# Performance work log

Measured on AMD Instinct MI355X. Metric: run time of the kernel, lower is better.

Reference implementation:

```python
import jax, jax.numpy as jnp
import numpy as np

N = 50000


def gcn_conv(x, ei, W, b, n_nodes):
    """PyG GCNConv with default add_self_loops=True, symmetric normalization."""
    h = x @ W  # [N, hidden]
    loop = jnp.arange(n_nodes, dtype=ei.dtype)
    src = jnp.concatenate([ei[0], loop])
    dst = jnp.concatenate([ei[1], loop])
    # degree over destination nodes, unit edge weights (incl. self loops)
    deg = jax.ops.segment_sum(jnp.ones(src.shape[0], dtype=h.dtype), dst, num_segments=n_nodes)
    dinv = jnp.where(deg > 0, jax.lax.rsqrt(deg), 0.0)
    norm = dinv[src] * dinv[dst]  # [E+N]
    out = jax.ops.segment_sum(norm[:, None] * h[src], dst, num_segments=n_nodes)
    return out + b


def setup_inputs() -> dict:
    key = jax.random.key(0)
    ks = jax.random.split(key, 16)
    d_in, hidden, d_out, E = 64, 64, 3, 800000
    inp = {
        "x": jax.random.normal(ks[0], (N, d_in), dtype=jnp.float32),
        "ei_spring": jax.random.randint(ks[1], (2, E), 0, N, dtype=jnp.int32),
        "ei_damper": jax.random.randint(ks[2], (2, E), 0, N, dtype=jnp.int32),
        "W1s": jax.random.normal(ks[3], (d_in, hidden), dtype=jnp.float32) / np.sqrt(d_in),
        "b1s": jnp.zeros((hidden,), dtype=jnp.float32),
        "W1d": jax.random.normal(ks[4], (d_in, hidden), dtype=jnp.float32) / np.sqrt(d_in),
        "b1d": jnp.zeros((hidden,), dtype=jnp.float32),
        "W2s": jax.random.normal(ks[5], (hidden, hidden), dtype=jnp.float32) / np.sqrt(hidden),
        "b2s": jnp.zeros((hidden,), dtype=jnp.float32),
        "W2d": jax.random.normal(ks[6], (hidden, hidden), dtype=jnp.float32) / np.sqrt(hidden),
        "b2d": jnp.zeros((hidden,), dtype=jnp.float32),
        "Wlin": jax.random.normal(ks[7], (hidden, d_out), dtype=jnp.float32) / np.sqrt(hidden),
        "blin": jnp.zeros((d_out,), dtype=jnp.float32),
    }
    return inp


def reference(x, ei_spring, ei_damper, W1s, b1s, W1d, b1d, W2s, b2s, W2d, b2d, Wlin, blin):
    # layer 1: HeteroConv sum over both relations, then ReLU
    h = gcn_conv(x, ei_spring, W1s, b1s, N) + gcn_conv(x, ei_damper, W1d, b1d, N)
    h = jax.nn.relu(h)
    # layer 2
    h = gcn_conv(h, ei_spring, W2s, b2s, N) + gcn_conv(h, ei_damper, W2d, b2d, N)
    h = jax.nn.relu(h)
    return h @ Wlin + blin
```

## Files before the change

kernel.cpp:

```cpp
#include <hip/hip_runtime.h>
#include <hip/hip_fp16.h>

#define NN 50000
#define BSHIFT 8
#define NBK ((NN + 255) >> 8)
#define CHUNK 4096
#define CAP 8192

typedef __attribute__((ext_vector_type(8))) _Float16 f16x8;
typedef __attribute__((ext_vector_type(4))) float f32x4;

__device__ __forceinline__ float recw(unsigned r) {
    unsigned short us = (unsigned short)(r >> 16);
    __half h;
    __builtin_memcpy(&h, &us, 2);
    return __half2float(h);
}
__device__ __forceinline__ float2 h2f2(unsigned v) {
    __half2 h;
    __builtin_memcpy(&h, &v, 4);
    return __half22float2(h);
}
__device__ __forceinline__ unsigned f2h2(float a, float b) {
    __half2 h = __floats2half2_rn(a, b);
    unsigned u;
    __builtin_memcpy(&u, &h, 4);
    return u;
}
__device__ __forceinline__ f16x8 as_f16x8(uint4 v) {
    f16x8 r;
    __builtin_memcpy(&r, &v, 16);
    return r;
}
__device__ __forceinline__ unsigned short f2h1(float v) {
    __half h = __float2half(v);
    unsigned short us;
    __builtin_memcpy(&us, &h, 2);
    return us;
}


__global__ __launch_bounds__(256) void fat_prep(const int* __restrict__ eiS, int Es,
                                                const int* __restrict__ eiD, int Ed,
                                                int* __restrict__ cntS,
                                                int* __restrict__ cntD,
                                                const float* __restrict__ x,
                                                unsigned* __restrict__ x16, int total4,
                                                const float* __restrict__ W1s,
                                                const float* __restrict__ W1d,
                                                const float* __restrict__ W2s,
                                                const float* __restrict__ W2d,
                                                unsigned short* __restrict__ Bp) {
    __shared__ int h[NBK];
    if (blockIdx.y < 2) {
        int rel = blockIdx.y;
        const int* dst = rel ? (eiD + Ed) : (eiS + Es);
        int E = rel ? Ed : Es;
        int* cnt = rel ? cntD : cntS;
        int base = blockIdx.x * CHUNK;
        if (base >= E) return;
        for (int i = threadIdx.x; i < NBK; i += 256) h[i] = 0;
        __syncthreads();
        int end = (base + CHUNK < E) ? base + CHUNK : E;
        for (int e = base + threadIdx.x; e < end; e += 256)
            atomicAdd(&h[dst[e] >> BSHIFT], 1);
        __syncthreads();
        for (int i = threadIdx.x; i < NBK; i += 256)
            if (h[i]) atomicAdd(&cnt[i], h[i]);
    } else {
        int i = blockIdx.x * 256 + threadIdx.x;
        if (i < total4) {
            float4 v = reinterpret_cast<const float4*>(x)[i];
            uint2 o;
            o.x = f2h2(v.x, v.y);
            o.y = f2h2(v.z, v.w);
            reinterpret_cast<uint2*>(x16)[i] = o;
        }
        if (blockIdx.x < 64) {
            int idx = blockIdx.x * 256 + threadIdx.x;
            int layer = idx >> 13;
            int rem = idx & 8191;
            int j = rem & 7;
            int l = (rem >> 3) & 63;
            int jt = (rem >> 9) & 3;
            int ks = rem >> 11;
            int k = ks * 32 + (l >> 4) * 8 + j;
            int col = jt * 16 + (l & 15);
            const float* Ws = layer ? W2s : W1s;
            const float* Wd = layer ? W2d : W1d;
            float v = (k < 64) ? Ws[k * 64 + col] : Wd[(k - 64) * 64 + col];
            Bp[idx] = f2h1(v);
        }
    }
}


__global__ __launch_bounds__(256) void bucket_scan(const int* __restrict__ cntS,
                                                   const int* __restrict__ cntD,
                                                   int* __restrict__ baseS,
                                                   int* __restrict__ baseD,
                                                   int* __restrict__ curS,
                                                   int* __restrict__ curD,
                                                   int* __restrict__ offsS,
                                                   int* __restrict__ offsD) {
    __shared__ int sA[256], sB[256];
    const int* cnt = blockIdx.x ? cntD : cntS;
    int* base = blockIdx.x ? baseD : baseS;
    int* cur  = blockIdx.x ? curD : curS;
    int* offs = blockIdx.x ? offsD : offsS;
    int t = threadIdx.x;
    int v = (t < NBK) ? cnt[t] : 0;
    sA[t] = v;
    __syncthreads();
    int* pin = sA; int* pout = sB;
    for (int st = 1; st < 256; st <<= 1) {
        int x = pin[t];
        if (t >= st) x += pin[t - st];
        pout[t] = x;
        __syncthreads();
        int* tmp = pin; pin = pout; pout = tmp;
    }
    int incl = pin[t];
    int excl = incl - v;
    if (t < NBK) { base[t] = excl; cur[t] = excl; }
    if (t == NBK - 1) { base[NBK] = incl; offs[NN] = incl; }
}


__global__ __launch_bounds__(256) void bucket_scatter(const int* __restrict__ eiS, int Es,
                                                      const int* __restrict__ eiD, int Ed,
                                                      int* __restrict__ curS,
                                                      int* __restrict__ curD,
                                                      unsigned* __restrict__ recS,
                                                      unsigned* __restrict__ recD) {
    __shared__ int h[NBK];
    __shared__ int rb[NBK];
    int rel = blockIdx.y;
    const int* ei = rel ? eiD : eiS;
    int E = rel ? Ed : Es;
    int* cur = rel ? curD : curS;
    unsigned* rec = rel ? recD : recS;
    int base = blockIdx.x * CHUNK;
    if (base >= E) return;
    const int* src = ei;
    const int* dst = ei + E;
    int end = (base + CHUNK < E) ? base + CHUNK : E;

    for (int i = threadIdx.x; i < NBK; i += 256) h[i] = 0;
    __syncthreads();
    for (int e = base + threadIdx.x; e < end; e += 256)
        atomicAdd(&h[dst[e] >> BSHIFT], 1);
    __syncthreads();
    for (int i = threadIdx.x; i < NBK; i += 256) {
        int c = h[i];
        rb[i] = c ? atomicAdd(&cur[i], c) : 0;
    }
    __syncthreads();
    for (int i = threadIdx.x; i < NBK; i += 256) h[i] = 0;
    __syncthreads();
    for (int e = base + threadIdx.x; e < end; e += 256) {
        int d = dst[e];
        int s = src[e];
        int b = d >> BSHIFT;
        int p = atomicAdd(&h[b], 1);
        rec[rb[b] + p] = (unsigned)s | ((unsigned)(d & 255) << 16);
    }
}


__global__ __launch_bounds__(256) void bucket_finalize(const int* __restrict__ baseS,
                                                       const int* __restrict__ baseD,
                                                       unsigned* __restrict__ recS,
                                                       unsigned* __restrict__ recD,
                                                       int* __restrict__ offsS,
                                                       int* __restrict__ offsD,
                                                       float* __restrict__ dinvS,
                                                       float* __restrict__ dinvD) {
    __shared__ unsigned recs[CAP];
    __shared__ int lc[256], sA[256], sB[256];
    int rel = blockIdx.y;
    const int* base = rel ? baseD : baseS;
    unsigned* rec = rel ? recD : recS;
    int* offs = rel ? offsD : offsS;
    float* dinv = rel ? dinvD : dinvS;
    int b = blockIdx.x;
    int b0 = base[b], b1 = base[b + 1];
    int cnt = b1 - b0;
    int t = threadIdx.x;
    lc[t] = 0;
    __syncthreads();
    for (int i = t; i < cnt; i += 256) {
        unsigned r = rec[b0 + i];
        if (i < CAP) recs[i] = r;
        atomicAdd(&lc[r >> 16], 1);
    }
    __syncthreads();
    int v = lc[t];
    int g = (b << BSHIFT) + t;
    if (g < NN) dinv[g] = rsqrtf((float)v + 1.0f);
    sA[t] = v;
    __syncthreads();
    int* pin = sA; int* pout = sB;
    for (int st = 1; st < 256; st <<= 1) {
        int x = pin[t];
        if (t >= st) x += pin[t - st];
        pout[t] = x;
        __syncthreads();
        int* tmp = pin; pin = pout; pout = tmp;
    }
    int excl = pin[t] - v;
    if (g < NN) offs[g] = b0 + excl;
    lc[t] = excl;
    __syncthreads();
    for (int i = t; i < cnt; i += 256) {
        unsigned r = (i < CAP) ? recs[i] : rec[b0 + i];
        int p = atomicAdd(&lc[r >> 16], 1);
        rec[b0 + p] = r & 0xFFFFu;
    }
}


__global__ __launch_bounds__(256) void pack_rec(unsigned* __restrict__ recS, int Es,
                                                unsigned* __restrict__ recD, int Ed,
                                                const float* __restrict__ dinvS,
                                                const float* __restrict__ dinvD) {
    int i = blockIdx.x * 256 + threadIdx.x;
    if (i < Es) {
        unsigned s = recS[i] & 0xFFFFu;
        recS[i] = s | ((unsigned)f2h1(dinvS[s]) << 16);
    }
    if (i < Ed) {
        unsigned s = recD[i] & 0xFFFFu;
        recD[i] = s | ((unsigned)f2h1(dinvD[s]) << 16);
    }
}


__global__ __launch_bounds__(256) void gather_agg(const int* __restrict__ offsS,
                                                  const unsigned* __restrict__ recS,
                                                  const int* __restrict__ offsD,
                                                  const unsigned* __restrict__ recD,
                                                  const unsigned* __restrict__ feat,
                                                  const float* __restrict__ dinvS,
                                                  const float* __restrict__ dinvD,
                                                  unsigned* __restrict__ A, int n) {
    int rel = blockIdx.y;
    const int* __restrict__ offs = rel ? offsD : offsS;
    const unsigned* __restrict__ rec = rel ? recD : recS;
    const float* __restrict__ dinv = rel ? dinvD : dinvS;

    int wv = (blockIdx.x * 256 + threadIdx.x) >> 6;
    int lane = threadIdx.x & 63;
    int c = lane >> 4;
    int q = lane & 15;
    int node = wv * 4 + c;
    if (node >= n) return;

    const uint2* featv = reinterpret_cast<const uint2*>(feat);

    float dv = dinv[node];
    int e0 = offs[node];
    int cnt = offs[node + 1] - e0;

    uint2 sv = featv[(size_t)node * 16 + q];
    float2 s0 = h2f2(sv.x), s1 = h2f2(sv.y);
    float a0 = dv * s0.x, a1 = dv * s0.y, a2 = dv * s1.x, a3 = dv * s1.y;

    int i = 0;
    while (__any(i < cnt)) {
#pragma unroll
        for (int k = 0; k < 4; k++) {
            int e = i + k;
            unsigned r = (e < cnt) ? rec[e0 + e] : 0u;
            uint2 v = featv[(size_t)(r & 0xFFFFu) * 16 + q];
            float wt = recw(r);
            float2 f0 = h2f2(v.x), f1 = h2f2(v.y);
            a0 = fmaf(wt, f0.x, a0);
            a1 = fmaf(wt, f0.y, a1);
            a2 = fmaf(wt, f1.x, a2);
            a3 = fmaf(wt, f1.y, a3);
        }
        i += 4;
    }

    uint2 o;
    o.x = f2h2(dv * a0, dv * a1);
    o.y = f2h2(dv * a2, dv * a3);
    reinterpret_cast<uint2*>(A)[(size_t)node * 32 + rel * 16 + q] = o;
}


#define STORE_JT(ACC, JT)                                                     \
    {                                                                         \
        int colj = (JT) * 16 + lr;                                            \
        float bs = ba[colj] + bb[colj];                                       \
        _Pragma("unroll")                                                     \
        for (int r = 0; r < 4; r++) {                                         \
            float v = fmaxf(ACC[r] + bs, 0.0f);                               \
            outH[(size_t)(m0 + lh * 4 + r) * 64 + colj] = f2h1(v);            \
        }                                                                     \
    }

#define HEAD_JT(ACC, JT)                                                      \
    {                                                                         \
        int colj = (JT) * 16 + lr;                                            \
        float bs = ba[colj] + bb[colj];                                       \
        float w0 = Wlin[colj * 3 + 0];                                        \
        float w1 = Wlin[colj * 3 + 1];                                        \
        float w2 = Wlin[colj * 3 + 2];                                        \
        _Pragma("unroll")                                                     \
        for (int r = 0; r < 4; r++) {                                         \
            float v = fmaxf(ACC[r] + bs, 0.0f);                               \
            h0[r] = fmaf(v, w0, h0[r]);                                       \
            h1[r] = fmaf(v, w1, h1[r]);                                       \
            h2[r] = fmaf(v, w2, h2[r]);                                       \
        }                                                                     \
    }

template <int HEAD>
__global__ __launch_bounds__(256) void apply_mfma(const unsigned* __restrict__ A,
                                                  const unsigned short* __restrict__ Bp,
                                                  const float* __restrict__ ba,
                                                  const float* __restrict__ bb,
                                                  const float* __restrict__ Wlin,
                                                  const float* __restrict__ blin,
                                                  unsigned short* __restrict__ outH,
                                                  float* __restrict__ out3, int n) {
    int wid = (blockIdx.x * 256 + threadIdx.x) >> 6;
    int l = threadIdx.x & 63;
    int m0 = wid * 16;
    if (m0 >= n) return;
    int lr = l & 15;
    int lh = l >> 4;

    const uint4* Bv = reinterpret_cast<const uint4*>(Bp);
    f32x4 acc0 = {0.f, 0.f, 0.f, 0.f};
    f32x4 acc1 = {0.f, 0.f, 0.f, 0.f};
    f32x4 acc2 = {0.f, 0.f, 0.f, 0.f};
    f32x4 acc3 = {0.f, 0.f, 0.f, 0.f};

#pragma unroll
    for (int ks = 0; ks < 4; ks++) {
        uint4 av = *reinterpret_cast<const uint4*>(A + (size_t)(m0 + lr) * 64 + ks * 16 + lh * 4);
        f16x8 af = as_f16x8(av);
        uint4 b0 = Bv[(ks * 4 + 0) * 64 + l];
        uint4 b1 = Bv[(ks * 4 + 1) * 64 + l];
        uint4 b2 = Bv[(ks * 4 + 2) * 64 + l];
        uint4 b3 = Bv[(ks * 4 + 3) * 64 + l];
        acc0 = __builtin_amdgcn_mfma_f32_16x16x32_f16(af, as_f16x8(b0), acc0, 0, 0, 0);
        acc1 = __builtin_amdgcn_mfma_f32_16x16x32_f16(af, as_f16x8(b1), acc1, 0, 0, 0);
        acc2 = __builtin_amdgcn_mfma_f32_16x16x32_f16(af, as_f16x8(b2), acc2, 0, 0, 0);
        acc3 = __builtin_amdgcn_mfma_f32_16x16x32_f16(af, as_f16x8(b3), acc3, 0, 0, 0);
    }

    if (HEAD == 0) {
        STORE_JT(acc0, 0)
        STORE_JT(acc1, 1)
        STORE_JT(acc2, 2)
        STORE_JT(acc3, 3)
    } else {
        float h0[4] = {0.f, 0.f, 0.f, 0.f};
        float h1[4] = {0.f, 0.f, 0.f, 0.f};
        float h2[4] = {0.f, 0.f, 0.f, 0.f};
        HEAD_JT(acc0, 0)
        HEAD_JT(acc1, 1)
        HEAD_JT(acc2, 2)
        HEAD_JT(acc3, 3)
#pragma unroll
        for (int st = 1; st < 16; st <<= 1) {
#pragma unroll
            for (int r = 0; r < 4; r++) {
                h0[r] += __shfl_xor(h0[r], st, 64);
                h1[r] += __shfl_xor(h1[r], st, 64);
                h2[r] += __shfl_xor(h2[r], st, 64);
            }
        }
        if (lr == 0) {
#pragma unroll
            for (int r = 0; r < 4; r++) {
                int row = m0 + lh * 4 + r;
                out3[row * 3 + 0] = h0[r] + blin[0];
                out3[row * 3 + 1] = h1[r] + blin[1];
                out3[row * 3 + 2] = h2[r] + blin[2];
            }
        }
    }
}

extern "C" void kernel_launch(void* const* d_in, const int* in_sizes, int n_in,
                              void* d_out, int out_size, void* d_ws, size_t ws_size,
                              hipStream_t stream) {
    const float* x    = (const float*)d_in[0];
    const int*   eis  = (const int*)d_in[1];
    const int*   eid  = (const int*)d_in[2];
    const float* W1s  = (const float*)d_in[3];
    const float* b1s  = (const float*)d_in[4];
    const float* W1d  = (const float*)d_in[5];
    const float* b1d  = (const float*)d_in[6];
    const float* W2s  = (const float*)d_in[7];
    const float* b2s  = (const float*)d_in[8];
    const float* W2d  = (const float*)d_in[9];
    const float* b2d  = (const float*)d_in[10];
    const float* Wlin = (const float*)d_in[11];
    const float* blin = (const float*)d_in[12];

    const int N  = NN;
    const int Es = in_sizes[1] / 2;
    const int Ed = in_sizes[2] / 2;
    int Emax = (Es > Ed) ? Es : Ed;

    int*   cntS  = (int*)d_ws;
    int*   cntD  = cntS + NBK;
    int*   baseS = cntD + NBK;
    int*   baseD = baseS + (NBK + 4);
    int*   curS  = baseD + (NBK + 4);
    int*   curD  = curS + NBK;
    int*   offsS = curD + NBK;
    int*   offsD = offsS + (N + 4);
    float* dinvS = (float*)(offsD + (N + 4));
    float* dinvD = dinvS + N;
    unsigned* recS = (unsigned*)(dinvD + N);
    unsigned* recD = recS + Es;
    unsigned* x16  = recD + Ed;
    unsigned* h16u = x16 + (size_t)N * 32;
    unsigned* Abuf = h16u + (size_t)N * 32;
    unsigned short* Bp = (unsigned short*)(Abuf + (size_t)N * 64);
    unsigned short* h16 = (unsigned short*)h16u;

    hipMemsetAsync(cntS, 0, (size_t)2 * NBK * sizeof(int), stream);
    dim3 pgrid(3125, 3);
    fat_prep<<<pgrid, 256, 0, stream>>>(eis, Es, eid, Ed, cntS, cntD,
                                        x, x16, N * 16, W1s, W1d, W2s, W2d, Bp);
    bucket_scan<<<2, 256, 0, stream>>>(cntS, cntD, baseS, baseD, curS, curD, offsS, offsD);
    dim3 egrid((Emax + CHUNK - 1) / CHUNK, 2);
    bucket_scatter<<<egrid, 256, 0, stream>>>(eis, Es, eid, Ed, curS, curD, recS, recD);
    dim3 fgrid(NBK, 2);
    bucket_finalize<<<fgrid, 256, 0, stream>>>(baseS, baseD, recS, recD, offsS, offsD,
                                               dinvS, dinvD);
    pack_rec<<<(Emax + 255) / 256, 256, 0, stream>>>(recS, Es, recD, Ed, dinvS, dinvD);

    dim3 ggrid((N + 15) / 16, 2);
    int mtiles = (N + 15) / 16;
    int applyBlocks = (mtiles * 64 + 255) / 256;

    gather_agg<<<ggrid, 256, 0, stream>>>(offsS, recS, offsD, recD, x16,
                                          dinvS, dinvD, Abuf, N);
    apply_mfma<0><<<applyBlocks, 256, 0, stream>>>(Abuf, Bp, b1s, b1d,
                                                   nullptr, nullptr, h16, nullptr, N);

    gather_agg<<<ggrid, 256, 0, stream>>>(offsS, recS, offsD, recD, h16u,
                                          dinvS, dinvD, Abuf, N);
    apply_mfma<1><<<applyBlocks, 256, 0, stream>>>(Abuf, Bp + 8192, b2s, b2d,
                                                   Wlin, blin, nullptr, (float*)d_out, N);
}
```

Measured before the change: 178.6 us.

## Split gather features into two column planes and software-pipeline edge record loads

Stores the fp16 node features (x16 and the layer-1 output) as two 32-column planes instead of one interleaved row. The aggregation kernel now runs one pass per plane, using 8 lanes per node and 8 nodes per wave, so each pass's randomly gathered working set is half the size and more likely to stay cache-resident. The edge loop is unrolled to 8 and prefetches the next 8 edge records with nontemporal loads, and the output is written with a nontemporal store. The cost is that every edge record and offset is read twice, once per pass, and more blocks are launched.

```diff
diff --git a/kernel.cpp b/kernel.cpp
--- a/kernel.cpp
+++ b/kernel.cpp
@@ -45,7 +45,7 @@
                                                 int* __restrict__ cntS,
                                                 int* __restrict__ cntD,
                                                 const float* __restrict__ x,
-                                                unsigned* __restrict__ x16, int total4,
+                                                unsigned* __restrict__ x16, int n,
                                                 const float* __restrict__ W1s,
                                                 const float* __restrict__ W1d,
                                                 const float* __restrict__ W2s,
@@ -69,12 +69,16 @@
             if (h[i]) atomicAdd(&cnt[i], h[i]);
     } else {
         int i = blockIdx.x * 256 + threadIdx.x;
-        if (i < total4) {
+        if (i < n * 16) {
             float4 v = reinterpret_cast<const float4*>(x)[i];
+            int node = i >> 4;
+            int ql = i & 15;
+            int plane = ql >> 3;
+            int q = ql & 7;
             uint2 o;
             o.x = f2h2(v.x, v.y);
             o.y = f2h2(v.z, v.w);
-            reinterpret_cast<uint2*>(x16)[i] = o;
+            reinterpret_cast<uint2*>(x16)[((size_t)plane * n + node) * 8 + q] = o;
         }
         if (blockIdx.x < 64) {
             int idx = blockIdx.x * 256 + threadIdx.x;
@@ -244,49 +248,68 @@
                                                   const float* __restrict__ dinvS,
                                                   const float* __restrict__ dinvD,
                                                   unsigned* __restrict__ A, int n) {
-    int rel = blockIdx.y;
+    int rel = blockIdx.y & 1;
+    int pass = blockIdx.y >> 1;
     const int* __restrict__ offs = rel ? offsD : offsS;
     const unsigned* __restrict__ rec = rel ? recD : recS;
     const float* __restrict__ dinv = rel ? dinvD : dinvS;
 
     int wv = (blockIdx.x * 256 + threadIdx.x) >> 6;
     int lane = threadIdx.x & 63;
-    int c = lane >> 4;
-    int q = lane & 15;
-    int node = wv * 4 + c;
+    int c = lane >> 3;
+    int q = lane & 7;
+    int node = wv * 8 + c;
     if (node >= n) return;
 
-    const uint2* featv = reinterpret_cast<const uint2*>(feat);
+    const uint2* __restrict__ featp =
+        reinterpret_cast<const uint2*>(feat) + (size_t)pass * n * 8;
 
     float dv = dinv[node];
     int e0 = offs[node];
     int cnt = offs[node + 1] - e0;
 
-    uint2 sv = featv[(size_t)node * 16 + q];
+    uint2 sv = featp[(size_t)node * 8 + q];
     float2 s0 = h2f2(sv.x), s1 = h2f2(sv.y);
     float a0 = dv * s0.x, a1 = dv * s0.y, a2 = dv * s1.x, a3 = dv * s1.y;
 
+    unsigned rn[8];
+#pragma unroll
+    for (int k = 0; k < 8; k++)
+        rn[k] = (k < cnt) ? __builtin_nontemporal_load(rec + e0 + k) : 0u;
+
     int i = 0;
     while (__any(i < cnt)) {
-#pragma unroll
-        for (int k = 0; k < 4; k++) {
-            int e = i + k;
-            unsigned r = (e < cnt) ? rec[e0 + e] : 0u;
-            uint2 v = featv[(size_t)(r & 0xFFFFu) * 16 + q];
-            float wt = recw(r);
-            float2 f0 = h2f2(v.x), f1 = h2f2(v.y);
+        unsigned rc[8];
+#pragma unroll
+        for (int k = 0; k < 8; k++) rc[k] = rn[k];
+        int j = i + 8;
+#pragma unroll
+        for (int k = 0; k < 8; k++)
+            rn[k] = (j + k < cnt) ? __builtin_nontemporal_load(rec + e0 + j + k) : 0u;
+        uint2 v[8];
+#pragma unroll
+        for (int k = 0; k < 8; k++)
+            v[k] = featp[(size_t)(rc[k] & 0xFFFFu) * 8 + q];
+#pragma unroll
+        for (int k = 0; k < 8; k++) {
+            float wt = recw(rc[k]);
+            float2 f0 = h2f2(v[k].x), f1 = h2f2(v[k].y);
             a0 = fmaf(wt, f0.x, a0);
             a1 = fmaf(wt, f0.y, a1);
             a2 = fmaf(wt, f1.x, a2);
             a3 = fmaf(wt, f1.y, a3);
         }
-        i += 4;
+        i = j;
     }
 
     uint2 o;
     o.x = f2h2(dv * a0, dv * a1);
     o.y = f2h2(dv * a2, dv * a3);
-    reinterpret_cast<uint2*>(A)[(size_t)node * 32 + rel * 16 + q] = o;
+    unsigned long long ov;
+    __builtin_memcpy(&ov, &o, 8);
+    unsigned long long* optr = reinterpret_cast<unsigned long long*>(
+        reinterpret_cast<uint2*>(A) + ((size_t)node * 32 + rel * 16 + pass * 8 + q));
+    __builtin_nontemporal_store(ov, optr);
 }
 
 
@@ -294,10 +317,11 @@
     {                                                                         \
         int colj = (JT) * 16 + lr;                                            \
         float bs = ba[colj] + bb[colj];                                       \
+        size_t pbase = (size_t)(colj >> 5) * n * 32 + (colj & 31);            \
         _Pragma("unroll")                                                     \
         for (int r = 0; r < 4; r++) {                                         \
             float v = fmaxf(ACC[r] + bs, 0.0f);                               \
-            outH[(size_t)(m0 + lh * 4 + r) * 64 + colj] = f2h1(v);            \
+            outH[pbase + (size_t)(m0 + lh * 4 + r) * 32] = f2h1(v);           \
         }                                                                     \
     }
 
@@ -430,7 +454,7 @@
     hipMemsetAsync(cntS, 0, (size_t)2 * NBK * sizeof(int), stream);
     dim3 pgrid(3125, 3);
     fat_prep<<<pgrid, 256, 0, stream>>>(eis, Es, eid, Ed, cntS, cntD,
-                                        x, x16, N * 16, W1s, W1d, W2s, W2d, Bp);
+                                        x, x16, N, W1s, W1d, W2s, W2d, Bp);
     bucket_scan<<<2, 256, 0, stream>>>(cntS, cntD, baseS, baseD, curS, curD, offsS, offsD);
     dim3 egrid((Emax + CHUNK - 1) / CHUNK, 2);
     bucket_scatter<<<egrid, 256, 0, stream>>>(eis, Es, eid, Ed, curS, curD, recS, recD);
@@ -439,7 +463,7 @@
                                                dinvS, dinvD);
     pack_rec<<<(Emax + 255) / 256, 256, 0, stream>>>(recS, Es, recD, Ed, dinvS, dinvD);
 
-    dim3 ggrid((N + 15) / 16, 2);
+    dim3 ggrid((N + 31) / 32, 4);
     int mtiles = (N + 15) / 16;
     int applyBlocks = (mtiles * 64 + 255) / 256;
 
```

Result: slower. 195.8 us (+9.6%).
